# Kernel tuning notes

Hardware: AMD Instinct MI355X
Metric: run time of the kernel (lower is better)

The kernel has to match this reference:

```python
import jax, jax.numpy as jnp
import numpy as np
from jax import lax

B, VLEN, H, DIM, C = 32, 2048, 1024, 1024, 32  # batch, value len, hidden_dim, dim, conv_out_channel


def setup_inputs() -> dict:
    key = jax.random.key(0)
    ks = jax.random.split(key, 13)
    s = 0.02
    return {
        "query": jax.random.normal(ks[0], (B, 1, H), dtype=jnp.float32),
        "value": jax.random.normal(ks[1], (B, VLEN, H), dtype=jnp.float32),
        "prev_attn": jax.random.uniform(ks[2], (B, VLEN), dtype=jnp.float32),
        "conv_w": jax.random.normal(ks[3], (C, 1, 3), dtype=jnp.float32) * s,   # Conv1d weight (out,in,k)
        "conv_b": jax.random.normal(ks[4], (C,), dtype=jnp.float32) * s,
        "w_loc": jax.random.normal(ks[5], (DIM, C), dtype=jnp.float32) * s,     # loc_projection (no bias)
        "w_q": jax.random.normal(ks[6], (DIM, H), dtype=jnp.float32) * s,       # query_projection (no bias)
        "w_v": jax.random.normal(ks[7], (DIM, H), dtype=jnp.float32) * s,       # value_projection (no bias)
        "bias": jax.random.uniform(ks[8], (DIM,), dtype=jnp.float32, minval=-0.1, maxval=0.1),
        "w_score": jax.random.normal(ks[9], (1, DIM), dtype=jnp.float32) * s,   # score_projection weight
        "b_score": jax.random.normal(ks[10], (1,), dtype=jnp.float32) * s,
        "w_out": jax.random.normal(ks[11], (H, 2 * H), dtype=jnp.float32) * s,  # out_projection weight
        "b_out": jax.random.normal(ks[12], (H,), dtype=jnp.float32) * s,
    }


def reference(query, value, prev_attn, conv_w, conv_b, w_loc, w_q, w_v, bias,
              w_score, b_score, w_out, b_out):
    # Location features: Conv1d(1 -> C, k=3, pad=1) over prev_attn, then transpose to (B, V, C)
    conv = lax.conv_general_dilated(
        prev_attn[:, None, :], conv_w, window_strides=(1,), padding=[(1, 1)],
        dimension_numbers=("NCH", "OIH", "NCH"),
    ) + conv_b[None, :, None]                       # (B, C, V)
    conv_feat = jnp.transpose(conv, (0, 2, 1))      # (B, V, C)

    qp = jnp.einsum("bqh,dh->bqd", query, w_q)      # (B, 1, DIM)
    vp = jnp.einsum("bvh,dh->bvd", value, w_v)      # (B, V, DIM)
    lp = jnp.einsum("bvc,dc->bvd", conv_feat, w_loc)

    e = jnp.tanh(qp + vp + lp + bias)               # (B, V, DIM), qp broadcasts over V
    score = jnp.einsum("bvd,d->bv", e, w_score[0]) + b_score[0]  # (B, V)

    # smoothing=True: sigmoid then normalize
    s = jax.nn.sigmoid(score)
    attn = s / jnp.sum(s, axis=-1, keepdims=True)   # (B, V)

    context = jnp.einsum("bv,bvh->bh", attn, value)               # (B, H)
    combined = jnp.concatenate([context[:, None, :], query], axis=2)  # (B, 1, 2H)
    output = jnp.einsum("bqk,hk->bqh", combined, w_out) + b_out       # (B, 1, H)
    return output, attn
```

## Files before the change

### kernel.cpp

```cpp
#include <hip/hip_runtime.h>
#include <hip/hip_bf16.h>
#include <math.h>

#define B_SZ 32
#define VLEN_SZ 2048
#define H_SZ 1024
#define DIM_SZ 1024
#define C_SZ 32

typedef float f32x4 __attribute__((ext_vector_type(4)));
typedef short s16x8 __attribute__((ext_vector_type(8)));
typedef short s16x4 __attribute__((ext_vector_type(4)));
typedef unsigned int u32x4 __attribute__((ext_vector_type(4)));

__device__ __forceinline__ short f2bf(float f) {
  unsigned u = __float_as_uint(f);
  u = (u + 0x7fffu + ((u >> 16) & 1u)) >> 16;
  return (short)u;
}

__device__ __forceinline__ float bf2f(short s) {
  return __uint_as_float(((unsigned)(unsigned short)s) << 16);
}

__device__ __forceinline__ unsigned pack2(float a, float b) {
  return __builtin_amdgcn_perm(__float_as_uint(b), __float_as_uint(a), 0x07060302u);
}

__device__ __forceinline__ float fast_tanh(float x) {
  float z = __expf(2.0f * x);
  return 1.0f - 2.0f / (z + 1.0f);
}

__device__ __forceinline__ void ldg_lds16(const void* g, void* l) {
  __builtin_amdgcn_global_load_lds(
      (const __attribute__((address_space(1))) unsigned int*)g,
      (__attribute__((address_space(3))) unsigned int*)l, 16, 0, 0);
}

__global__ __launch_bounds__(256) void k_prep(
    const float* __restrict__ query, const float* __restrict__ w_q,
    const float* __restrict__ bias, const float* __restrict__ prev,
    const float* __restrict__ conv_w, const float* __restrict__ conv_b,
    const float* __restrict__ w_loc, const float* __restrict__ w_v,
    const float* __restrict__ value,
    float* __restrict__ qpb, short* __restrict__ cfb, short* __restrict__ wlocb,
    short* __restrict__ wvb, short* __restrict__ vb,
    float* __restrict__ score, float* __restrict__ context) {
  int bid = blockIdx.x;
  int t = threadIdx.x;
  if (bid < 8192) {
    int wid = bid * 4 + (t >> 6);
    int lane = t & 63;
    int d = wid >> 5;
    int b = wid & 31;
    const f32x4* q4 = (const f32x4*)(query + (size_t)b * H_SZ);
    const f32x4* w4 = (const f32x4*)(w_q + (size_t)d * H_SZ);
    float acc = 0.f;
#pragma unroll
    for (int it = 0; it < 4; ++it) {
      int k = it * 64 + lane;
      f32x4 a = q4[k], w = w4[k];
      acc += a[0] * w[0] + a[1] * w[1] + a[2] * w[2] + a[3] * w[3];
    }
#pragma unroll
    for (int off = 32; off; off >>= 1) acc += __shfl_xor(acc, off, 64);
    if (lane == 0) qpb[(size_t)b * DIM_SZ + d] = acc + bias[d];
  } else if (bid < 8448) {
    int r = (bid - 8192) * 256 + t;
    int v = r & (VLEN_SZ - 1);
    float p0 = prev[r];
    float pm = (v > 0) ? prev[r - 1] : 0.f;
    float pp = (v < VLEN_SZ - 1) ? prev[r + 1] : 0.f;
    float o[C_SZ];
#pragma unroll
    for (int c = 0; c < C_SZ; ++c)
      o[c] = conv_b[c] + pm * conv_w[c * 3 + 0] + p0 * conv_w[c * 3 + 1] + pp * conv_w[c * 3 + 2];
    s16x8* dst = (s16x8*)(cfb + (size_t)r * C_SZ);
#pragma unroll
    for (int g = 0; g < 4; ++g) {
      s16x8 pk;
#pragma unroll
      for (int e = 0; e < 8; ++e) pk[e] = f2bf(o[8 * g + e]);
      dst[g] = pk;
    }
  } else if (bid < 8480) {
    int i = (bid - 8448) * 256 + t;
    f32x4 v = ((const f32x4*)w_loc)[i];
    s16x4 o;
    o[0] = f2bf(v[0]); o[1] = f2bf(v[1]); o[2] = f2bf(v[2]); o[3] = f2bf(v[3]);
    ((s16x4*)wlocb)[i] = o;
  } else if (bid < 9504) {
    int i = (bid - 8480) * 256 + t;
    f32x4 v = ((const f32x4*)w_v)[i];
    s16x4 o;
    o[0] = f2bf(v[0]); o[1] = f2bf(v[1]); o[2] = f2bf(v[2]); o[3] = f2bf(v[3]);
    ((s16x4*)wvb)[i] = o;
  } else if (bid < 9568) {
    int i = (bid - 9504) * 256 + t;
    ((f32x4*)score)[i] = (f32x4){0.f, 0.f, 0.f, 0.f};
  } else if (bid < 9600) {
    int i = (bid - 9568) * 256 + t;
    ((f32x4*)context)[i] = (f32x4){0.f, 0.f, 0.f, 0.f};
  } else {
    size_t i = (size_t)(bid - 9600) * 256 + t;
    const f32x4* src = (const f32x4*)value;
    f32x4 v0 = src[2 * i], v1 = src[2 * i + 1];
    s16x8 o;
    o[0] = f2bf(v0[0]); o[1] = f2bf(v0[1]); o[2] = f2bf(v0[2]); o[3] = f2bf(v0[3]);
    o[4] = f2bf(v1[0]); o[5] = f2bf(v1[1]); o[6] = f2bf(v1[2]); o[7] = f2bf(v1[3]);
    ((s16x8*)vb)[i] = o;
  }
}

__global__ __launch_bounds__(256, 4) void k_score(
    const short* __restrict__ vb, const short* __restrict__ wvb,
    const short* __restrict__ wlocb, const short* __restrict__ cfb,
    const float* __restrict__ qpb, const float* __restrict__ w_score,
    float* __restrict__ score) {
  __shared__ short As[128 * 32];
  __shared__ short Bs[128 * 32];
  __shared__ float sred[4][64];

  int t = threadIdx.x;
  int w = t >> 6, l = t & 63;
  int q = l >> 4, l16 = l & 15;
  int bid = blockIdx.x;
  int x = bid & 7;
  int j = bid >> 3;
  int nt = j & 7;
  int mt = x * 64 + (j >> 3);
  int row0 = mt * 128;
  int d0 = nt * 128;
  int b = row0 >> 11;
  int wm = w >> 1, wn = w & 1;

  int lr = l >> 2;
  int kc = ((l & 3) ^ ((l >> 3) & 3)) * 8;
  const short* gA0 = vb + (size_t)(row0 + 32 * w + lr) * H_SZ + kc;
  const short* gA1 = vb + (size_t)(row0 + 32 * w + 16 + lr) * H_SZ + kc;
  const short* gB0 = wvb + (size_t)(d0 + 32 * w + lr) * H_SZ + kc;
  const short* gB1 = wvb + (size_t)(d0 + 32 * w + 16 + lr) * H_SZ + kc;
  short* lA0 = As + (32 * w) * 32;
  short* lA1 = As + (32 * w + 16) * 32;
  short* lB0 = Bs + (32 * w) * 32;
  short* lB1 = Bs + (32 * w + 16) * 32;

  int posf = (q ^ ((l16 >> 1) & 3)) * 8;

  f32x4 acc[4][4];
#pragma unroll
  for (int i = 0; i < 4; ++i)
#pragma unroll
    for (int jj = 0; jj < 4; ++jj) acc[i][jj] = (f32x4){0.f, 0.f, 0.f, 0.f};

  for (int kt = 0; kt <= 32; ++kt) {
    if (kt < 32) {
      int k0 = kt * 32;
      ldg_lds16(gA0 + k0, lA0);
      ldg_lds16(gA1 + k0, lA1);
      ldg_lds16(gB0 + k0, lB0);
      ldg_lds16(gB1 + k0, lB1);
    } else {
      ldg_lds16(cfb + (size_t)(row0 + 32 * w + lr) * C_SZ + kc, lA0);
      ldg_lds16(cfb + (size_t)(row0 + 32 * w + 16 + lr) * C_SZ + kc, lA1);
      ldg_lds16(wlocb + (size_t)(d0 + 32 * w + lr) * C_SZ + kc, lB0);
      ldg_lds16(wlocb + (size_t)(d0 + 32 * w + 16 + lr) * C_SZ + kc, lB1);
    }
    __syncthreads();

    s16x8 a[4], bb[4];
#pragma unroll
    for (int i = 0; i < 4; ++i)
      a[i] = *(const s16x8*)(As + (wm * 64 + i * 16 + l16) * 32 + posf);
#pragma unroll
    for (int jj = 0; jj < 4; ++jj)
      bb[jj] = *(const s16x8*)(Bs + (wn * 64 + jj * 16 + l16) * 32 + posf);
#pragma unroll
    for (int i = 0; i < 4; ++i)
#pragma unroll
      for (int jj = 0; jj < 4; ++jj)
        acc[i][jj] = __builtin_amdgcn_mfma_f32_16x16x32_bf16(a[i], bb[jj], acc[i][jj], 0, 0, 0);
    __syncthreads();
  }

  float qv[4], wv[4];
#pragma unroll
  for (int jj = 0; jj < 4; ++jj) {
    int d = d0 + wn * 64 + jj * 16 + l16;
    qv[jj] = qpb[(size_t)b * DIM_SZ + d];
    wv[jj] = w_score[d];
  }

#pragma unroll
  for (int i = 0; i < 4; ++i) {
#pragma unroll
    for (int r = 0; r < 4; ++r) {
      float part = 0.f;
#pragma unroll
      for (int jj = 0; jj < 4; ++jj)
        part += fast_tanh(acc[i][jj][r] + qv[jj]) * wv[jj];
      part += __shfl_xor(part, 1);
      part += __shfl_xor(part, 2);
      part += __shfl_xor(part, 4);
      part += __shfl_xor(part, 8);
      if (l16 == 0) sred[w][i * 16 + q * 4 + r] = part;
    }
  }
  __syncthreads();
  if (t < 128) {
    int half = t >> 6;
    float v = sred[half * 2][t & 63] + sred[half * 2 + 1][t & 63];
    atomicAdd(&score[row0 + t], v);
  }
}

__global__ __launch_bounds__(256) void k_prep_f32(
    const float* __restrict__ query, const float* __restrict__ w_q,
    const float* __restrict__ bias, const float* __restrict__ prev,
    const float* __restrict__ conv_w, const float* __restrict__ conv_b,
    const float* __restrict__ w_loc, const float* __restrict__ w_v,
    float* __restrict__ qpb, float* __restrict__ cff, short* __restrict__ wlocb,
    short* __restrict__ wvb, float* __restrict__ score, float* __restrict__ context) {
  int bid = blockIdx.x;
  int t = threadIdx.x;
  if (bid < 8192) {
    int wid = bid * 4 + (t >> 6);
    int lane = t & 63;
    int d = wid >> 5;
    int b = wid & 31;
    const f32x4* q4 = (const f32x4*)(query + (size_t)b * H_SZ);
    const f32x4* w4 = (const f32x4*)(w_q + (size_t)d * H_SZ);
    float acc = 0.f;
#pragma unroll
    for (int it = 0; it < 4; ++it) {
      int k = it * 64 + lane;
      f32x4 a = q4[k], w = w4[k];
      acc += a[0] * w[0] + a[1] * w[1] + a[2] * w[2] + a[3] * w[3];
    }
#pragma unroll
    for (int off = 32; off; off >>= 1) acc += __shfl_xor(acc, off, 64);
    if (lane == 0) qpb[(size_t)b * DIM_SZ + d] = acc + bias[d];
  } else if (bid < 8448) {
    int r = (bid - 8192) * 256 + t;
    int v = r & (VLEN_SZ - 1);
    float p0 = prev[r];
    float pm = (v > 0) ? prev[r - 1] : 0.f;
    float pp = (v < VLEN_SZ - 1) ? prev[r + 1] : 0.f;
    float o[C_SZ];
#pragma unroll
    for (int c = 0; c < C_SZ; ++c)
      o[c] = conv_b[c] + pm * conv_w[c * 3 + 0] + p0 * conv_w[c * 3 + 1] + pp * conv_w[c * 3 + 2];
    f32x4* dst = (f32x4*)(cff + (size_t)r * C_SZ);
#pragma unroll
    for (int g = 0; g < 8; ++g)
      dst[g] = (f32x4){o[4 * g], o[4 * g + 1], o[4 * g + 2], o[4 * g + 3]};
  } else if (bid < 8480) {
    int i = (bid - 8448) * 256 + t;
    f32x4 v = ((const f32x4*)w_loc)[i];
    s16x4 o;
    o[0] = f2bf(v[0]); o[1] = f2bf(v[1]); o[2] = f2bf(v[2]); o[3] = f2bf(v[3]);
    ((s16x4*)wlocb)[i] = o;
  } else if (bid < 9504) {
    int i = (bid - 8480) * 256 + t;
    f32x4 v = ((const f32x4*)w_v)[i];
    s16x4 o;
    o[0] = f2bf(v[0]); o[1] = f2bf(v[1]); o[2] = f2bf(v[2]); o[3] = f2bf(v[3]);
    ((s16x4*)wvb)[i] = o;
  } else if (bid < 9568) {
    int i = (bid - 9504) * 256 + t;
    ((f32x4*)score)[i] = (f32x4){0.f, 0.f, 0.f, 0.f};
  } else {
    int i = (bid - 9568) * 256 + t;
    ((f32x4*)context)[i] = (f32x4){0.f, 0.f, 0.f, 0.f};
  }
}

__global__ __launch_bounds__(256, 4) void k_score_f32(
    const float* __restrict__ value, const short* __restrict__ wvb,
    const short* __restrict__ wlocb, const float* __restrict__ cff,
    const float* __restrict__ qpb, const float* __restrict__ w_score,
    float* __restrict__ score) {
  __shared__ float As[128 * 32];
  __shared__ short Bs[128 * 32];
  __shared__ float sred[4][64];

  int t = threadIdx.x;
  int w = t >> 6, l = t & 63;
  int q = l >> 4, l16 = l & 15;
  int bid = blockIdx.x;
  int x = bid & 7;
  int j = bid >> 3;
  int nt = j & 7;
  int mt = x * 64 + (j >> 3);
  int row0 = mt * 128;
  int d0 = nt * 128;
  int b = row0 >> 11;
  int wm = w >> 1, wn = w & 1;

  int ar = l >> 3;
  int ac = (l & 7) ^ ar;
  const float* gA[4];
  float* lA[4];
#pragma unroll
  for (int s = 0; s < 4; ++s) {
    gA[s] = value + (size_t)(row0 + 32 * w + 8 * s + ar) * H_SZ + ac * 4;
    lA[s] = As + (32 * w + 8 * s) * 32;
  }
  int lr = l >> 2;
  int kc = ((l & 3) ^ ((l >> 3) & 3)) * 8;
  const short* gB0 = wvb + (size_t)(d0 + 32 * w + lr) * H_SZ + kc;
  const short* gB1 = wvb + (size_t)(d0 + 32 * w + 16 + lr) * H_SZ + kc;
  short* lB0 = Bs + (32 * w) * 32;
  short* lB1 = Bs + (32 * w + 16) * 32;

  int h7 = l16 & 7;
  int pA0 = ((2 * q) ^ h7) * 4;
  int pA1 = ((2 * q + 1) ^ h7) * 4;
  int posB = (q ^ ((l16 >> 1) & 3)) * 8;

  f32x4 acc[4][4];
#pragma unroll
  for (int i = 0; i < 4; ++i)
#pragma unroll
    for (int jj = 0; jj < 4; ++jj) acc[i][jj] = (f32x4){0.f, 0.f, 0.f, 0.f};

  for (int kt = 0; kt <= 32; ++kt) {
    if (kt < 32) {
      int k0 = kt * 32;
#pragma unroll
      for (int s = 0; s < 4; ++s) ldg_lds16(gA[s] + k0, lA[s]);
      ldg_lds16(gB0 + (size_t)k0, lB0);
      ldg_lds16(gB1 + (size_t)k0, lB1);
    } else {
#pragma unroll
      for (int s = 0; s < 4; ++s)
        ldg_lds16(cff + (size_t)(row0 + 32 * w + 8 * s + ar) * C_SZ + ac * 4, lA[s]);
      ldg_lds16(wlocb + (size_t)(d0 + 32 * w + lr) * C_SZ + kc, lB0);
      ldg_lds16(wlocb + (size_t)(d0 + 32 * w + 16 + lr) * C_SZ + kc, lB1);
    }
    __syncthreads();

    s16x8 a[4], bb[4];
#pragma unroll
    for (int i = 0; i < 4; ++i) {
      const float* rowp = As + (wm * 64 + i * 16 + l16) * 32;
      f32x4 f0 = *(const f32x4*)(rowp + pA0);
      f32x4 f1 = *(const f32x4*)(rowp + pA1);
      u32x4 pk;
      pk[0] = pack2(f0[0], f0[1]);
      pk[1] = pack2(f0[2], f0[3]);
      pk[2] = pack2(f1[0], f1[1]);
      pk[3] = pack2(f1[2], f1[3]);
      a[i] = *(s16x8*)&pk;
    }
#pragma unroll
    for (int jj = 0; jj < 4; ++jj)
      bb[jj] = *(const s16x8*)(Bs + (wn * 64 + jj * 16 + l16) * 32 + posB);
#pragma unroll
    for (int i = 0; i < 4; ++i)
#pragma unroll
      for (int jj = 0; jj < 4; ++jj)
        acc[i][jj] = __builtin_amdgcn_mfma_f32_16x16x32_bf16(a[i], bb[jj], acc[i][jj], 0, 0, 0);
    __syncthreads();
  }

  float qv[4], wv[4];
#pragma unroll
  for (int jj = 0; jj < 4; ++jj) {
    int d = d0 + wn * 64 + jj * 16 + l16;
    qv[jj] = qpb[(size_t)b * DIM_SZ + d];
    wv[jj] = w_score[d];
  }

#pragma unroll
  for (int i = 0; i < 4; ++i) {
#pragma unroll
    for (int r = 0; r < 4; ++r) {
      float part = 0.f;
#pragma unroll
      for (int jj = 0; jj < 4; ++jj)
        part += fast_tanh(acc[i][jj][r] + qv[jj]) * wv[jj];
      part += __shfl_xor(part, 1);
      part += __shfl_xor(part, 2);
      part += __shfl_xor(part, 4);
      part += __shfl_xor(part, 8);
      if (l16 == 0) sred[w][i * 16 + q * 4 + r] = part;
    }
  }
  __syncthreads();
  if (t < 128) {
    int half = t >> 6;
    float v = sred[half * 2][t & 63] + sred[half * 2 + 1][t & 63];
    atomicAdd(&score[row0 + t], v);
  }
}

__global__ __launch_bounds__(256) void k_ctx(
    const float* __restrict__ score, const float* __restrict__ b_score,
    const float* __restrict__ value, float* __restrict__ attn_out,
    float* __restrict__ context) {
  __shared__ float als[VLEN_SZ];
  __shared__ float red[4];
  int b = blockIdx.x, vc = blockIdx.y, t = threadIdx.x;
  float bs = b_score[0];
  float sv[8];
  float lsum = 0.f;
  int v0 = t * 8;
#pragma unroll
  for (int k = 0; k < 8; ++k) {
    float ps = score[(size_t)b * VLEN_SZ + v0 + k] + bs;
    float s = 1.0f / (1.0f + __expf(-ps));
    sv[k] = s;
    lsum += s;
    als[v0 + k] = s;
  }
#pragma unroll
  for (int off = 32; off; off >>= 1) lsum += __shfl_xor(lsum, off, 64);
  if ((t & 63) == 0) red[t >> 6] = lsum;
  __syncthreads();
  float inv = 1.0f / (red[0] + red[1] + red[2] + red[3]);
  if (vc == 0) {
#pragma unroll
    for (int k = 0; k < 8; ++k)
      attn_out[(size_t)b * VLEN_SZ + v0 + k] = sv[k] * inv;
  }

  int h0 = t * 4;
  int vbase = vc * 128;
  const float* vp = value + ((size_t)b * VLEN_SZ + vbase) * H_SZ + h0;
  const float* av = als + vbase;
  f32x4 acc = (f32x4){0.f, 0.f, 0.f, 0.f};
#pragma unroll 8
  for (int v = 0; v < 128; ++v) {
    f32x4 xv = *(const f32x4*)(vp + (size_t)v * H_SZ);
    float a = av[v];
    acc[0] += a * xv[0]; acc[1] += a * xv[1];
    acc[2] += a * xv[2]; acc[3] += a * xv[3];
  }
#pragma unroll
  for (int k = 0; k < 4; ++k)
    atomicAdd(&context[(size_t)b * H_SZ + h0 + k], acc[k] * inv);
}

__global__ void k_out(const float* __restrict__ context, const float* __restrict__ query,
                      const float* __restrict__ w_out, const float* __restrict__ b_out,
                      float* __restrict__ out) {
  int wid = blockIdx.x * 4 + (threadIdx.x >> 6);
  int lane = threadIdx.x & 63;
  int h = wid >> 5;
  int b = wid & 31;
  const f32x4* w4 = (const f32x4*)(w_out + (size_t)h * 2048);
  const f32x4* c4 = (const f32x4*)(context + (size_t)b * H_SZ);
  const f32x4* q4 = (const f32x4*)(query + (size_t)b * H_SZ);
  float acc = 0.f;
#pragma unroll
  for (int it = 0; it < 8; ++it) {
    int k4 = it * 64 + lane;
    f32x4 w = w4[k4];
    f32x4 c = (k4 < 256) ? c4[k4] : q4[k4 - 256];
    acc += w[0] * c[0] + w[1] * c[1] + w[2] * c[2] + w[3] * c[3];
  }
#pragma unroll
  for (int off = 32; off; off >>= 1) acc += __shfl_xor(acc, off, 64);
  if (lane == 0) out[(size_t)b * H_SZ + h] = acc + b_out[h];
}

extern "C" void kernel_launch(void* const* d_in, const int* in_sizes, int n_in,
                              void* d_out, int out_size, void* d_ws, size_t ws_size,
                              hipStream_t stream) {
  const float* query   = (const float*)d_in[0];
  const float* value   = (const float*)d_in[1];
  const float* prev    = (const float*)d_in[2];
  const float* conv_w  = (const float*)d_in[3];
  const float* conv_b  = (const float*)d_in[4];
  const float* w_loc   = (const float*)d_in[5];
  const float* w_q     = (const float*)d_in[6];
  const float* w_v     = (const float*)d_in[7];
  const float* bias    = (const float*)d_in[8];
  const float* w_score = (const float*)d_in[9];
  const float* b_score = (const float*)d_in[10];
  const float* w_out   = (const float*)d_in[11];
  const float* b_out   = (const float*)d_in[12];

  float* out  = (float*)d_out;
  float* attn = out + B_SZ * H_SZ;

  char* ws = (char*)d_ws;
  float* score   = (float*)(ws);
  float* qpb     = (float*)(ws + (256 << 10));
  float* context = (float*)(ws + (384 << 10));
  short* wvb     = (short*)(ws + (512 << 10));
  short* wlocb   = (short*)(ws + (2560 << 10));

  size_t need = ((size_t)16 << 20) + ((size_t)128 << 20);
  if (ws_size >= need) {
    short* cfb = (short*)(ws + (3 << 20));
    short* vb  = (short*)(ws + ((size_t)16 << 20));
    k_prep<<<42368, 256, 0, stream>>>(query, w_q, bias, prev, conv_w, conv_b,
                                      w_loc, w_v, value, qpb, cfb, wlocb, wvb, vb,
                                      score, context);
    k_score<<<4096, 256, 0, stream>>>(vb, wvb, wlocb, cfb, qpb, w_score, score);
  } else {
    float* cff = (float*)(ws + (3 << 20));
    k_prep_f32<<<9600, 256, 0, stream>>>(query, w_q, bias, prev, conv_w, conv_b,
                                         w_loc, w_v, qpb, cff, wlocb, wvb, score, context);
    k_score_f32<<<4096, 256, 0, stream>>>(value, wvb, wlocb, cff, qpb, w_score, score);
  }
  k_ctx<<<dim3(B_SZ, 16), 256, 0, stream>>>(score, b_score, value, attn, context);
  k_out<<<(B_SZ * H_SZ) / 4, 256, 0, stream>>>(context, query, w_out, b_out, out);
}
```

Before: 657.9 us.

## Use 256x256 tiles with triple-buffered LDS pipeline and bf16 value in context

Replaces the 128x128 score GEMM kernel with a 512-thread 256x256-tile kernel. It triple-buffers LDS, prefetches global-to-LDS two k-steps ahead, splits the MFMA work into half-phases around barriers, and raises wave priority during MFMA. This aims to raise data reuse per tile and overlap loads with compute. The context kernel now reads the bf16 copy of value instead of fp32, halving that traffic, at the cost of some precision in the context sum.

```diff
diff --git a/kernel.cpp b/kernel.cpp
--- a/kernel.cpp
+++ b/kernel.cpp
@@ -113,93 +113,125 @@
   }
 }
 
-__global__ __launch_bounds__(256, 4) void k_score(
+#define STAGE_A(ktv, bi_)                                                    \
+  do {                                                                       \
+    const short* s0_ = ((ktv) < 32) ? aBaseV + (size_t)(ktv) * 32 : aBaseC;  \
+    const short* s1_ = ((ktv) < 32) ? aBaseV + (size_t)(ktv) * 32 + 131072   \
+                                    : aBaseC + 4096;                         \
+    ldg_lds16(s0_, ldw + (bi_) * 16384);                                     \
+    ldg_lds16(s1_, ldw + (bi_) * 16384 + 4096);                              \
+  } while (0)
+
+#define STAGE_B(ktv, bi_)                                                    \
+  do {                                                                       \
+    const short* s0_ = ((ktv) < 32) ? bBaseV + (size_t)(ktv) * 32 : bBaseC;  \
+    const short* s1_ = ((ktv) < 32) ? bBaseV + (size_t)(ktv) * 32 + 131072   \
+                                    : bBaseC + 4096;                         \
+    ldg_lds16(s0_, ldw + (bi_) * 16384 + 8192);                              \
+    ldg_lds16(s1_, ldw + (bi_) * 16384 + 12288);                             \
+  } while (0)
+
+__global__ __launch_bounds__(512, 2) void k_score8(
     const short* __restrict__ vb, const short* __restrict__ wvb,
     const short* __restrict__ wlocb, const short* __restrict__ cfb,
     const float* __restrict__ qpb, const float* __restrict__ w_score,
     float* __restrict__ score) {
-  __shared__ short As[128 * 32];
-  __shared__ short Bs[128 * 32];
-  __shared__ float sred[4][64];
+  __shared__ short lds_s[3 * 16384];
+  __shared__ float sred[8][128];
 
   int t = threadIdx.x;
   int w = t >> 6, l = t & 63;
   int q = l >> 4, l16 = l & 15;
+  int wm = w >> 2, wn = w & 3;
   int bid = blockIdx.x;
-  int x = bid & 7;
-  int j = bid >> 3;
-  int nt = j & 7;
-  int mt = x * 64 + (j >> 3);
-  int row0 = mt * 128;
-  int d0 = nt * 128;
+  int x = bid & 7, j = bid >> 3;
+  int nt = j & 3, mt = x * 32 + (j >> 2);
+  int row0 = mt * 256, d0 = nt * 256;
   int b = row0 >> 11;
-  int wm = w >> 1, wn = w & 1;
-
-  int lr = l >> 2;
-  int kc = ((l & 3) ^ ((l >> 3) & 3)) * 8;
-  const short* gA0 = vb + (size_t)(row0 + 32 * w + lr) * H_SZ + kc;
-  const short* gA1 = vb + (size_t)(row0 + 32 * w + 16 + lr) * H_SZ + kc;
-  const short* gB0 = wvb + (size_t)(d0 + 32 * w + lr) * H_SZ + kc;
-  const short* gB1 = wvb + (size_t)(d0 + 32 * w + 16 + lr) * H_SZ + kc;
-  short* lA0 = As + (32 * w) * 32;
-  short* lA1 = As + (32 * w + 16) * 32;
-  short* lB0 = Bs + (32 * w) * 32;
-  short* lB1 = Bs + (32 * w + 16) * 32;
+
+  int ar = l >> 2;
+  int cc = ((l & 3) ^ ((l >> 3) & 3)) * 8;
+  int roff = w * 16 + ar;
+  const short* aBaseV = vb + (size_t)(row0 + roff) * H_SZ + cc;
+  const short* bBaseV = wvb + (size_t)(d0 + roff) * H_SZ + cc;
+  const short* aBaseC = cfb + (size_t)(row0 + roff) * C_SZ + cc;
+  const short* bBaseC = wlocb + (size_t)(d0 + roff) * C_SZ + cc;
+  short* ldw = lds_s + w * 512;
 
   int posf = (q ^ ((l16 >> 1) & 3)) * 8;
 
-  f32x4 acc[4][4];
-#pragma unroll
-  for (int i = 0; i < 4; ++i)
-#pragma unroll
-    for (int jj = 0; jj < 4; ++jj) acc[i][jj] = (f32x4){0.f, 0.f, 0.f, 0.f};
-
-  for (int kt = 0; kt <= 32; ++kt) {
-    if (kt < 32) {
-      int k0 = kt * 32;
-      ldg_lds16(gA0 + k0, lA0);
-      ldg_lds16(gA1 + k0, lA1);
-      ldg_lds16(gB0 + k0, lB0);
-      ldg_lds16(gB1 + k0, lB1);
-    } else {
-      ldg_lds16(cfb + (size_t)(row0 + 32 * w + lr) * C_SZ + kc, lA0);
-      ldg_lds16(cfb + (size_t)(row0 + 32 * w + 16 + lr) * C_SZ + kc, lA1);
-      ldg_lds16(wlocb + (size_t)(d0 + 32 * w + lr) * C_SZ + kc, lB0);
-      ldg_lds16(wlocb + (size_t)(d0 + 32 * w + 16 + lr) * C_SZ + kc, lB1);
-    }
-    __syncthreads();
-
-    s16x8 a[4], bb[4];
-#pragma unroll
-    for (int i = 0; i < 4; ++i)
-      a[i] = *(const s16x8*)(As + (wm * 64 + i * 16 + l16) * 32 + posf);
-#pragma unroll
-    for (int jj = 0; jj < 4; ++jj)
-      bb[jj] = *(const s16x8*)(Bs + (wn * 64 + jj * 16 + l16) * 32 + posf);
-#pragma unroll
-    for (int i = 0; i < 4; ++i)
-#pragma unroll
-      for (int jj = 0; jj < 4; ++jj)
-        acc[i][jj] = __builtin_amdgcn_mfma_f32_16x16x32_bf16(a[i], bb[jj], acc[i][jj], 0, 0, 0);
-    __syncthreads();
+  f32x4 acc[8][4];
+#pragma unroll
+  for (int i = 0; i < 8; ++i)
+#pragma unroll
+    for (int n = 0; n < 4; ++n) acc[i][n] = (f32x4){0.f, 0.f, 0.f, 0.f};
+
+  STAGE_A(0, 0); STAGE_B(0, 0);
+  STAGE_A(1, 1); STAGE_B(1, 1);
+  asm volatile("s_waitcnt vmcnt(4)" ::: "memory");
+  __builtin_amdgcn_s_barrier();
+
+  int bi = 0, bs = 2;
+  for (int kt = 0; kt < 33; ++kt) {
+    const short* As = lds_s + bi * 16384;
+    const short* Bs = As + 8192;
+    bool st = (kt <= 30);
+
+    s16x8 af[4], bf[4];
+#pragma unroll
+    for (int m = 0; m < 4; ++m)
+      af[m] = *(const s16x8*)(As + (wm * 128 + m * 16 + l16) * 32 + posf);
+#pragma unroll
+    for (int n = 0; n < 4; ++n)
+      bf[n] = *(const s16x8*)(Bs + (wn * 64 + n * 16 + l16) * 32 + posf);
+    if (st) STAGE_A(kt + 2, bs);
+    __builtin_amdgcn_s_barrier();
+    __builtin_amdgcn_s_setprio(1);
+#pragma unroll
+    for (int m = 0; m < 4; ++m)
+#pragma unroll
+      for (int n = 0; n < 4; ++n)
+        acc[m][n] = __builtin_amdgcn_mfma_f32_16x16x32_bf16(af[m], bf[n], acc[m][n], 0, 0, 0);
+    __builtin_amdgcn_s_setprio(0);
+    __builtin_amdgcn_s_barrier();
+
+#pragma unroll
+    for (int m = 0; m < 4; ++m)
+      af[m] = *(const s16x8*)(As + (wm * 128 + (m + 4) * 16 + l16) * 32 + posf);
+    if (st) STAGE_B(kt + 2, bs);
+    __builtin_amdgcn_s_barrier();
+    __builtin_amdgcn_s_setprio(1);
+#pragma unroll
+    for (int m = 0; m < 4; ++m)
+#pragma unroll
+      for (int n = 0; n < 4; ++n)
+        acc[m + 4][n] = __builtin_amdgcn_mfma_f32_16x16x32_bf16(af[m], bf[n], acc[m + 4][n], 0, 0, 0);
+    __builtin_amdgcn_s_setprio(0);
+    if (kt < 31) {
+      asm volatile("s_waitcnt vmcnt(4)" ::: "memory");
+    } else if (kt == 31) {
+      asm volatile("s_waitcnt vmcnt(0)" ::: "memory");
+    }
+    __builtin_amdgcn_s_barrier();
+    bi = (bi == 2) ? 0 : bi + 1;
+    bs = (bs == 2) ? 0 : bs + 1;
   }
 
   float qv[4], wv[4];
 #pragma unroll
-  for (int jj = 0; jj < 4; ++jj) {
-    int d = d0 + wn * 64 + jj * 16 + l16;
-    qv[jj] = qpb[(size_t)b * DIM_SZ + d];
-    wv[jj] = w_score[d];
-  }
-
-#pragma unroll
-  for (int i = 0; i < 4; ++i) {
+  for (int n = 0; n < 4; ++n) {
+    int d = d0 + wn * 64 + n * 16 + l16;
+    qv[n] = qpb[(size_t)b * DIM_SZ + d];
+    wv[n] = w_score[d];
+  }
+#pragma unroll
+  for (int i = 0; i < 8; ++i) {
 #pragma unroll
     for (int r = 0; r < 4; ++r) {
       float part = 0.f;
 #pragma unroll
-      for (int jj = 0; jj < 4; ++jj)
-        part += fast_tanh(acc[i][jj][r] + qv[jj]) * wv[jj];
+      for (int n = 0; n < 4; ++n)
+        part += fast_tanh(acc[i][n][r] + qv[n]) * wv[n];
       part += __shfl_xor(part, 1);
       part += __shfl_xor(part, 2);
       part += __shfl_xor(part, 4);
@@ -208,9 +240,10 @@
     }
   }
   __syncthreads();
-  if (t < 128) {
-    int half = t >> 6;
-    float v = sred[half * 2][t & 63] + sred[half * 2 + 1][t & 63];
+  if (t < 256) {
+    int wmh = t >> 7, lr = t & 127;
+    float v = sred[wmh * 4][lr] + sred[wmh * 4 + 1][lr] +
+              sred[wmh * 4 + 2][lr] + sred[wmh * 4 + 3][lr];
     atomicAdd(&score[row0 + t], v);
   }
 }
@@ -398,6 +431,53 @@
 
 __global__ __launch_bounds__(256) void k_ctx(
     const float* __restrict__ score, const float* __restrict__ b_score,
+    const short* __restrict__ vb, float* __restrict__ attn_out,
+    float* __restrict__ context) {
+  __shared__ float als[VLEN_SZ];
+  __shared__ float red[4];
+  int b = blockIdx.x, vc = blockIdx.y, t = threadIdx.x;
+  float bs = b_score[0];
+  float sv[8];
+  float lsum = 0.f;
+  int v0 = t * 8;
+#pragma unroll
+  for (int k = 0; k < 8; ++k) {
+    float ps = score[(size_t)b * VLEN_SZ + v0 + k] + bs;
+    float s = 1.0f / (1.0f + __expf(-ps));
+    sv[k] = s;
+    lsum += s;
+    als[v0 + k] = s;
+  }
+#pragma unroll
+  for (int off = 32; off; off >>= 1) lsum += __shfl_xor(lsum, off, 64);
+  if ((t & 63) == 0) red[t >> 6] = lsum;
+  __syncthreads();
+  float inv = 1.0f / (red[0] + red[1] + red[2] + red[3]);
+  if (vc == 0) {
+#pragma unroll
+    for (int k = 0; k < 8; ++k)
+      attn_out[(size_t)b * VLEN_SZ + v0 + k] = sv[k] * inv;
+  }
+
+  int h0 = t * 4;
+  int vbase = vc * 128;
+  const short* vp = vb + ((size_t)b * VLEN_SZ + vbase) * H_SZ + h0;
+  const float* av = als + vbase;
+  f32x4 acc = (f32x4){0.f, 0.f, 0.f, 0.f};
+#pragma unroll 8
+  for (int v = 0; v < 128; ++v) {
+    s16x4 xv = *(const s16x4*)(vp + (size_t)v * H_SZ);
+    float a = av[v];
+    acc[0] += a * bf2f(xv[0]); acc[1] += a * bf2f(xv[1]);
+    acc[2] += a * bf2f(xv[2]); acc[3] += a * bf2f(xv[3]);
+  }
+#pragma unroll
+  for (int k = 0; k < 4; ++k)
+    atomicAdd(&context[(size_t)b * H_SZ + h0 + k], acc[k] * inv);
+}
+
+__global__ __launch_bounds__(256) void k_ctx_f32(
+    const float* __restrict__ score, const float* __restrict__ b_score,
     const float* __restrict__ value, float* __restrict__ attn_out,
     float* __restrict__ context) {
   __shared__ float als[VLEN_SZ];
@@ -500,13 +580,14 @@
     k_prep<<<42368, 256, 0, stream>>>(query, w_q, bias, prev, conv_w, conv_b,
                                       w_loc, w_v, value, qpb, cfb, wlocb, wvb, vb,
                                       score, context);
-    k_score<<<4096, 256, 0, stream>>>(vb, wvb, wlocb, cfb, qpb, w_score, score);
+    k_score8<<<1024, 512, 0, stream>>>(vb, wvb, wlocb, cfb, qpb, w_score, score);
+    k_ctx<<<dim3(B_SZ, 16), 256, 0, stream>>>(score, b_score, vb, attn, context);
   } else {
     float* cff = (float*)(ws + (3 << 20));
     k_prep_f32<<<9600, 256, 0, stream>>>(query, w_q, bias, prev, conv_w, conv_b,
                                          w_loc, w_v, qpb, cff, wlocb, wvb, score, context);
     k_score_f32<<<4096, 256, 0, stream>>>(value, wvb, wlocb, cff, qpb, w_score, score);
-  }
-  k_ctx<<<dim3(B_SZ, 16), 256, 0, stream>>>(score, b_score, value, attn, context);
+    k_ctx_f32<<<dim3(B_SZ, 16), 256, 0, stream>>>(score, b_score, value, attn, context);
+  }
   k_out<<<(B_SZ * H_SZ) / 4, 256, 0, stream>>>(context, query, w_out, b_out, out);
 }
```

After: 648.0 us. About the same (-1.5%).
